# Optimization experiments

Measured on AMD Instinct MI355X. Metric: run time of the kernel, lower is better.

The kernel has to match this reference:

```python
import jax, jax.numpy as jnp
import numpy as np

NT = 128          # num_timesteps (reference query points)
E = 128           # embed_time
H = 128           # nhidden
NH = 1            # num_heads
F = 32            # feature_size
NS = 2            # num_states
EPS = 1e-5


def layer_norm(x, g, b):
    m = jnp.mean(x, axis=-1, keepdims=True)
    v = jnp.mean((x - m) ** 2, axis=-1, keepdims=True)
    return (x - m) * jax.lax.rsqrt(v + EPS) * g + b


def setup_inputs() -> dict:
    key = jax.random.key(0)
    ks = jax.random.split(key, 24)
    nrm = lambda k, s: (jax.random.normal(k, s) * 0.05).astype(jnp.float32)
    inp = {
        "input": jax.random.normal(ks[0], (8, F, 512), dtype=jnp.float32),
        "mask": jax.random.randint(ks[1], (8, F, 512), 0, 2).astype(jnp.float32),
        "timesteps": jnp.sort(jax.random.uniform(ks[2], (8, 512), dtype=jnp.float32), axis=-1),
        # time embedding
        "periodic_w": nrm(ks[3], (E - 1, 1)), "periodic_b": nrm(ks[4], (E - 1,)),
        "lin_w": nrm(ks[5], (1, 1)), "lin_b": nrm(ks[6], (1,)),
        # query / key projections + layer norms
        "q_w": nrm(ks[7], (E, E)), "q_b": nrm(ks[8], (E,)),
        "q_g": jnp.ones((E,), jnp.float32), "q_be": jnp.zeros((E,), jnp.float32),
        "k_w": nrm(ks[9], (E, E)), "k_b": nrm(ks[10], (E,)),
        "k_g": jnp.ones((E,), jnp.float32), "k_be": jnp.zeros((E,), jnp.float32),
        # attention_norm over h*2F channels, then output linear + LN to nhidden
        "attn_g": jnp.ones((NH * 2 * F,), jnp.float32), "attn_b": jnp.zeros((NH * 2 * F,), jnp.float32),
        "out_w": nrm(ks[11], (H, NH * 2 * F)), "out_b": nrm(ks[12], (H,)),
        "out_g": jnp.ones((H,), jnp.float32), "out_be": jnp.zeros((H,), jnp.float32),
        # GRU (torch gate order r, z, n)
        "gru_wih": nrm(ks[13], (3 * H, H)), "gru_whh": nrm(ks[14], (3 * H, H)),
        "gru_bih": nrm(ks[15], (3 * H,)), "gru_bhh": nrm(ks[16], (3 * H,)),
        # classifier MLP
        "c1_w": nrm(ks[17], (H, H)), "c1_b": nrm(ks[18], (H,)),
        "c2_w": nrm(ks[19], (H, H)), "c2_b": nrm(ks[20], (H,)),
        "c3_w": nrm(ks[21], (NS, H)), "c3_b": nrm(ks[22], (NS,)),
    }
    return inp


def time_embedding(tt, lin_w, lin_b, periodic_w, periodic_b):
    t = tt[..., None]                                   # (..., 1)
    out1 = t @ lin_w.T + lin_b                          # (..., 1)
    out2 = jnp.sin(t @ periodic_w.T + periodic_b)       # (..., E-1)
    return jnp.concatenate([out1, out2], axis=-1)       # (..., E)


def reference(input, mask, timesteps, periodic_w, periodic_b, lin_w, lin_b,
              q_w, q_b, q_g, q_be, k_w, k_b, k_g, k_be,
              attn_g, attn_b, out_w, out_b, out_g, out_be,
              gru_wih, gru_whh, gru_bih, gru_bhh,
              c1_w, c1_b, c2_w, c2_b, c3_w, c3_b):
    B = input.shape[0]
    x_in = jnp.transpose(input, (0, 2, 1))              # (B, T, F)
    m = 1.0 - jnp.transpose(mask, (0, 2, 1))            # (B, T, F)
    x_in = x_in * (m > 0).astype(x_in.dtype)
    x = jnp.concatenate([x_in, m], axis=-1)             # (B, T, 2F)
    mk = jnp.concatenate([m, m], axis=-1)               # (B, T, 2F)

    key_e = time_embedding(timesteps, lin_w, lin_b, periodic_w, periodic_b)        # (B, T, E)
    qtimes = jnp.linspace(0.0, 1.0, NT)
    query_e = time_embedding(qtimes[None], lin_w, lin_b, periodic_w, periodic_b)   # (1, NT, E)

    q = layer_norm(query_e @ q_w.T + q_b, q_g, q_be)    # (1, NT, E)
    k = layer_norm(key_e @ k_w.T + k_b, k_g, k_be)      # (B, T, E)

    etk = E // NH
    q = q.reshape(1, NT, NH, etk).transpose(0, 2, 1, 3)         # (1, h, NT, etk)
    k = k.reshape(B, -1, NH, etk).transpose(0, 2, 1, 3)         # (B, h, T, etk)

    scores = jnp.einsum("ahqd,bhkd->bhqk", q, k) / np.sqrt(etk)  # (B, h, NT, T)
    # per-channel masked softmax over keys: (B, h, NT, T, 2F)
    logits = jnp.where(mk[:, None, None, :, :] == 0, -1e9, scores[..., None])
    p_attn = jax.nn.softmax(logits, axis=-2)
    att = jnp.sum(p_attn * x[:, None, None, :, :], axis=-2)     # (B, h, NT, 2F)

    x2 = att.transpose(0, 2, 1, 3).reshape(B, NT, NH * 2 * F)
    x2 = layer_norm(x2, attn_g, attn_b)
    out = layer_norm(x2 @ out_w.T + out_b, out_g, out_be)       # (B, NT, H)

    # GRU over the NT reference timesteps, last hidden state
    seq = out.transpose(1, 0, 2)                                # (NT, B, H)
    h0 = jnp.zeros((B, H), out.dtype)

    def gru_step(h, x_t):
        gi = x_t @ gru_wih.T + gru_bih
        gh = h @ gru_whh.T + gru_bhh
        ir, iz, inn = jnp.split(gi, 3, axis=-1)
        hr, hz, hn = jnp.split(gh, 3, axis=-1)
        r = jax.nn.sigmoid(ir + hr)
        z = jax.nn.sigmoid(iz + hz)
        n = jnp.tanh(inn + r * hn)
        h_new = (1.0 - z) * n + z * h
        return h_new, None

    h_last, _ = jax.lax.scan(gru_step, h0, seq)

    h1 = jax.nn.relu(h_last @ c1_w.T + c1_b)
    h2 = jax.nn.relu(h1 @ c2_w.T + c2_b)
    return h2 @ c3_w.T + c3_b                                   # (B, num_states) logits
```

## Files before the change

kernel.cpp:

```cpp
#include <hip/hip_runtime.h>
#include <math.h>

#define LN_EPS 1e-5f

typedef _Float16 h2v __attribute__((ext_vector_type(2)));

__device__ __forceinline__ float dot4(float4 a, float4 b) {
    return a.x*b.x + a.y*b.y + a.z*b.z + a.w*b.w;
}
__device__ __forceinline__ float fast_sigmoid(float x) {
    return 1.f / (1.f + __expf(-x));
}
__device__ __forceinline__ float fast_tanh(float x) {
    const float e = __expf(2.f * x);
    return 1.f - 2.f / (e + 1.f);
}
__device__ __forceinline__ float fdot2u(unsigned int a, unsigned int b, float c) {
#if __has_builtin(__builtin_amdgcn_fdot2)
    return __builtin_amdgcn_fdot2(__builtin_bit_cast(h2v, a),
                                  __builtin_bit_cast(h2v, b), c, false);
#else
    const h2v av = __builtin_bit_cast(h2v, a);
    const h2v bv = __builtin_bit_cast(h2v, b);
    return c + (float)av[0]*(float)bv[0] + (float)av[1]*(float)bv[1];
#endif
}
__device__ __forceinline__ float wsum64(float v) {
    #pragma unroll
    for (int off = 32; off > 0; off >>= 1) v += __shfl_xor(v, off);
    return v;
}

__global__ void k_embed_proj(
    const float* __restrict__ input, const float* __restrict__ mask,
    const float* __restrict__ timesteps,
    const float* __restrict__ pw, const float* __restrict__ pb,
    const float* __restrict__ lw, const float* __restrict__ lb,
    const float* __restrict__ q_w, const float* __restrict__ q_b,
    const float* __restrict__ q_g, const float* __restrict__ q_be,
    const float* __restrict__ k_w, const float* __restrict__ k_b,
    const float* __restrict__ k_g, const float* __restrict__ k_be,
    float* __restrict__ qs, float* __restrict__ kT, float2* __restrict__ xm)
{
    const int blk = blockIdx.x;
    const int tid = threadIdx.x;

    __shared__ __align__(16) float e[4][128];
    __shared__ __align__(16) float4 red[128];
    __shared__ __align__(16) float proj[4][128];
    __shared__ __align__(16) float2 tile[32][65];

    if (blk >= 1056) {
        const int b  = blk - 1056;
        const int cg = tid >> 6;
        const int tt = tid & 63;
        for (int t0 = 0; t0 < 512; t0 += 64) {
            for (int c16 = 0; c16 < 16; ++c16) {
                const int c = c16*2 + cg;
                const float m = mask [(size_t)(b*32 + c)*512 + t0 + tt];
                const float x = input[(size_t)(b*32 + c)*512 + t0 + tt];
                const float mm = 1.0f - m;
                tile[c][tt] = make_float2(x*mm, mm);
            }
            __syncthreads();
            const int c2 = tid & 31;
            const int tg = tid >> 5;
            #pragma unroll
            for (int k = 0; k < 16; ++k) {
                const int t = tg*16 + k;
                xm[((size_t)b*512 + t0 + t)*32 + c2] = tile[c2][t];
            }
            __syncthreads();
        }
        return;
    }

    const bool isq = blk < 32;
    float tv[4];
    int kidx0 = 0;
    if (isq) {
        const int q0 = blk * 4;
        #pragma unroll
        for (int r = 0; r < 4; ++r) tv[r] = (float)(q0 + r) * (1.0f/127.0f);
    } else {
        kidx0 = (blk - 32) * 4;
        #pragma unroll
        for (int r = 0; r < 4; ++r) tv[r] = timesteps[kidx0 + r];
    }

    float pwj = 0.f, pbj = 0.f;
    if (tid > 0) { pwj = pw[tid-1]; pbj = pb[tid-1]; }
    const float lw0 = lw[0], lb0 = lb[0];
    #pragma unroll
    for (int r = 0; r < 4; ++r)
        e[r][tid] = (tid == 0) ? (tv[r]*lw0 + lb0) : sinf(tv[r]*pwj + pbj);
    __syncthreads();

    const float* W  = isq ? q_w  : k_w;
    const float* Bv = isq ? q_b  : k_b;
    const float* G  = isq ? q_g  : k_g;
    const float* Be = isq ? q_be : k_be;

    {
        const int jj = tid >> 2, dc = tid & 3;
        const float4* e0 = (const float4*)(&e[0][0]);
        const float4* e1 = (const float4*)(&e[1][0]);
        const float4* e2 = (const float4*)(&e[2][0]);
        const float4* e3 = (const float4*)(&e[3][0]);
        #pragma unroll
        for (int jb = 0; jb < 4; ++jb) {
            const int j = jb*32 + jj;
            const float4* wrow = (const float4*)(W + (size_t)j*128);
            float a0=0.f, a1=0.f, a2=0.f, a3=0.f;
            #pragma unroll
            for (int k = 0; k < 8; ++k) {
                const int idx = dc + 4*k;
                const float4 w4 = wrow[idx];
                a0 += dot4(w4, e0[idx]);
                a1 += dot4(w4, e1[idx]);
                a2 += dot4(w4, e2[idx]);
                a3 += dot4(w4, e3[idx]);
            }
            a0 += __shfl_xor(a0, 1, 4); a0 += __shfl_xor(a0, 2, 4);
            a1 += __shfl_xor(a1, 1, 4); a1 += __shfl_xor(a1, 2, 4);
            a2 += __shfl_xor(a2, 1, 4); a2 += __shfl_xor(a2, 2, 4);
            a3 += __shfl_xor(a3, 1, 4); a3 += __shfl_xor(a3, 2, 4);
            if (dc == 0) {
                const float bj = Bv[j];
                proj[0][j] = a0 + bj; proj[1][j] = a1 + bj;
                proj[2][j] = a2 + bj; proj[3][j] = a3 + bj;
            }
        }
    }
    __syncthreads();

    float acc[4];
    #pragma unroll
    for (int r = 0; r < 4; ++r) acc[r] = proj[r][tid];

    red[tid] = make_float4(acc[0], acc[1], acc[2], acc[3]);
    __syncthreads();
    for (int s = 64; s > 0; s >>= 1) {
        if (tid < s) {
            float4 m = red[tid]; const float4 o = red[tid+s];
            m.x += o.x; m.y += o.y; m.z += o.z; m.w += o.w;
            red[tid] = m;
        }
        __syncthreads();
    }
    float4 mean = red[0];
    mean.x *= (1.0f/128.0f); mean.y *= (1.0f/128.0f);
    mean.z *= (1.0f/128.0f); mean.w *= (1.0f/128.0f);
    __syncthreads();
    const float d0 = acc[0]-mean.x, d1 = acc[1]-mean.y,
                d2 = acc[2]-mean.z, d3 = acc[3]-mean.w;
    red[tid] = make_float4(d0*d0, d1*d1, d2*d2, d3*d3);
    __syncthreads();
    for (int s = 64; s > 0; s >>= 1) {
        if (tid < s) {
            float4 m = red[tid]; const float4 o = red[tid+s];
            m.x += o.x; m.y += o.y; m.z += o.z; m.w += o.w;
            red[tid] = m;
        }
        __syncthreads();
    }
    float4 var = red[0];
    var.x *= (1.0f/128.0f); var.y *= (1.0f/128.0f);
    var.z *= (1.0f/128.0f); var.w *= (1.0f/128.0f);

    const float gg = G[tid], bb = Be[tid];
    const float o0 = d0*rsqrtf(var.x+LN_EPS)*gg + bb;
    const float o1 = d1*rsqrtf(var.y+LN_EPS)*gg + bb;
    const float o2 = d2*rsqrtf(var.z+LN_EPS)*gg + bb;
    const float o3 = d3*rsqrtf(var.w+LN_EPS)*gg + bb;

    if (isq) {
        const float sc = 0.08838834764831845f;
        const int q0 = blk*4;
        qs[(size_t)(q0+0)*128 + tid] = o0*sc;
        qs[(size_t)(q0+1)*128 + tid] = o1*sc;
        qs[(size_t)(q0+2)*128 + tid] = o2*sc;
        qs[(size_t)(q0+3)*128 + tid] = o3*sc;
    } else {
        const int b = kidx0 >> 9;
        const int t = kidx0 & 511;
        *(float4*)(kT + ((size_t)(b*128 + tid))*512 + t) =
            make_float4(o0, o1, o2, o3);
    }
}

__global__ void __launch_bounds__(256) k_attn(
    const float2* __restrict__ xm,
    const float* __restrict__ qs, const float* __restrict__ kT,
    const float* __restrict__ attn_g, const float* __restrict__ attn_b,
    const float* __restrict__ out_w, const float* __restrict__ out_b,
    const float* __restrict__ out_g, const float* __restrict__ out_be,
    float* __restrict__ outm)
{
    const int b     = blockIdx.x >> 5;
    const int qbase = (blockIdx.x & 31) * 4;
    const int tid   = threadIdx.x;

    __shared__ __align__(16) float et[4][512];
    __shared__ __align__(16) float qsh[4][128];
    __shared__ __align__(16) float wsh[128*66];
    __shared__ __align__(16) float sA[4][8][32];
    __shared__ __align__(16) float aA[4][8][32];
    __shared__ __align__(16) float x2s[4][64];
    __shared__ float redC[4];

    for (int idx = tid; idx < 512; idx += 256)
        qsh[idx >> 7][idx & 127] = qs[(size_t)(qbase + (idx >> 7))*128 + (idx & 127)];
    for (int idx = tid; idx < 8192; idx += 256)
        wsh[(idx >> 6)*66 + (idx & 63)] = out_w[idx];
    __syncthreads();

    {
        const int grp = tid >> 7;
        const int tl  = tid & 127;
        const int q0  = grp*2;
        const float4* kp = (const float4*)kT + (size_t)b*128*128 + tl;
        float4 a0 = make_float4(0,0,0,0), a1 = make_float4(0,0,0,0);
        for (int d = 0; d < 128; ++d) {
            const float4 kv = kp[(size_t)d*128];
            const float qa = qsh[q0][d], qb = qsh[q0+1][d];
            a0.x += qa*kv.x; a0.y += qa*kv.y; a0.z += qa*kv.z; a0.w += qa*kv.w;
            a1.x += qb*kv.x; a1.y += qb*kv.y; a1.z += qb*kv.z; a1.w += qb*kv.w;
        }
        a0.x = __expf(a0.x); a0.y = __expf(a0.y); a0.z = __expf(a0.z); a0.w = __expf(a0.w);
        a1.x = __expf(a1.x); a1.y = __expf(a1.y); a1.z = __expf(a1.z); a1.w = __expf(a1.w);
        ((float4*)et[q0])[tl]   = a0;
        ((float4*)et[q0+1])[tl] = a1;
    }
    __syncthreads();

    {
        const int c   = tid & 31;
        const int seg = tid >> 5;
        const float2* xp = xm + ((size_t)b*512 + seg*64)*32 + c;
        float s0=0,s1=0,s2=0,s3=0, a0=0,a1=0,a2=0,a3=0;
        #pragma unroll 4
        for (int i = 0; i < 64; ++i) {
            const float2 v = xp[(size_t)i*32];
            const int t = seg*64 + i;
            const float w0 = et[0][t]*v.y, w1 = et[1][t]*v.y;
            const float w2 = et[2][t]*v.y, w3 = et[3][t]*v.y;
            s0 += w0; s1 += w1; s2 += w2; s3 += w3;
            a0 += w0*v.x; a1 += w1*v.x; a2 += w2*v.x; a3 += w3*v.x;
        }
        sA[0][seg][c]=s0; sA[1][seg][c]=s1; sA[2][seg][c]=s2; sA[3][seg][c]=s3;
        aA[0][seg][c]=a0; aA[1][seg][c]=a1; aA[2][seg][c]=a2; aA[3][seg][c]=a3;
    }
    __syncthreads();

    {
        const int ql = tid >> 6;
        const int c2 = tid & 63;
        const int cc = c2 & 31;
        float ss = 0.f;
        #pragma unroll
        for (int g = 0; g < 8; ++g) ss += sA[ql][g][cc];
        float attv;
        if (c2 < 32) {
            float aa = 0.f;
            #pragma unroll
            for (int g = 0; g < 8; ++g) aa += aA[ql][g][cc];
            attv = (ss > 0.f) ? aa/ss : 0.f;
        } else {
            attv = (ss > 0.f) ? 1.0f : 0.0f;
        }
        const float mean = wsum64(attv) * (1.0f/64.0f);
        const float dv = attv - mean;
        const float var = wsum64(dv*dv) * (1.0f/64.0f);
        x2s[ql][c2] = dv*rsqrtf(var+LN_EPS)*attn_g[c2] + attn_b[c2];
    }
    __syncthreads();

    {
        const int jhalf = tid >> 7;
        const int j     = tid & 127;
        const int wave  = tid >> 6;
        for (int lq2 = 0; lq2 < 2; ++lq2) {
            const int ql = jhalf*2 + lq2;
            float acc = out_b[j];
            const float4* wrow = (const float4*)(wsh + j*66);
            const float4* xr   = (const float4*)x2s[ql];
            #pragma unroll
            for (int k = 0; k < 16; ++k) acc += dot4(wrow[k], xr[k]);

            float v = wsum64(acc);
            if ((tid & 63) == 0) redC[wave] = v;
            __syncthreads();
            const float mean = (redC[jhalf*2] + redC[jhalf*2+1]) * (1.0f/128.0f);
            __syncthreads();
            const float d = acc - mean;
            v = wsum64(d*d);
            if ((tid & 63) == 0) redC[wave] = v;
            __syncthreads();
            const float var = (redC[jhalf*2] + redC[jhalf*2+1]) * (1.0f/128.0f);
            outm[((size_t)b*128 + qbase + ql)*128 + j] =
                d*rsqrtf(var+LN_EPS)*out_g[j] + out_be[j];
            __syncthreads();
        }
    }
}

__global__ void k_gi(const float* __restrict__ outm,
                     const float* __restrict__ wih, const float* __restrict__ bih,
                     float* __restrict__ gi)
{
    const int qi  = blockIdx.x;
    const int tid = threadIdx.x;
    __shared__ __align__(16) float rows[8][128];
    for (int idx = tid; idx < 1024; idx += 384) {
        const int b = idx >> 7, d = idx & 127;
        rows[b][d] = outm[(size_t)(b*128+qi)*128 + d];
    }
    __syncthreads();

    const int g0 = tid >> 2, dc = tid & 3;
    #pragma unroll
    for (int gb = 0; gb < 4; ++gb) {
        const int g = gb*96 + g0;
        const float4* wrow = (const float4*)(wih + (size_t)g*128);
        float acc[8] = {0,0,0,0,0,0,0,0};
        #pragma unroll
        for (int k = 0; k < 8; ++k) {
            const int idx = dc + 4*k;
            const float4 w4 = wrow[idx];
            #pragma unroll
            for (int b = 0; b < 8; ++b)
                acc[b] += dot4(w4, ((const float4*)rows[b])[idx]);
        }
        #pragma unroll
        for (int b = 0; b < 8; ++b) {
            acc[b] += __shfl_xor(acc[b], 1, 4);
            acc[b] += __shfl_xor(acc[b], 2, 4);
        }
        if (dc == 0) {
            const float bi = bih[g];
            #pragma unroll
            for (int b = 0; b < 8; ++b)
                gi[((size_t)qi*8 + b)*384 + g] = acc[b] + bi;
        }
    }
}

__global__ void __launch_bounds__(512) k_gru_cls(
    const float* __restrict__ gi,
    const float* __restrict__ whh, const float* __restrict__ bhh,
    const float* __restrict__ c1w, const float* __restrict__ c1b,
    const float* __restrict__ c2w, const float* __restrict__ c2b,
    const float* __restrict__ c3w, const float* __restrict__ c3b,
    float* __restrict__ out)
{
    const int b   = blockIdx.x;
    const int tid = threadIdx.x;
    const int s   = tid >> 7;
    const int u   = tid & 127;

    __shared__ __align__(16) unsigned int lds[25344];
    unsigned int* hP  = lds;
    float* part = (float*)&lds[64];
    float* hcls = (float*)&lds[1216];

    {
        const float4* w4 = (const float4*)whh;
        #pragma unroll 4
        for (int k = 0; k < 24; ++k) {
            const int idx = tid + k*512;
            const float4 v = w4[idx];
            const int row = idx >> 5, c4 = idx & 31;
            h2v p0; p0[0] = (_Float16)v.x; p0[1] = (_Float16)v.y;
            h2v p1; p1[0] = (_Float16)v.z; p1[1] = (_Float16)v.w;
            lds[row*66 + c4*2    ] = __builtin_bit_cast(unsigned int, p0);
            lds[row*66 + c4*2 + 1] = __builtin_bit_cast(unsigned int, p1);
        }
    }
    __syncthreads();

    unsigned int wreg[3][16];
    #pragma unroll
    for (int g = 0; g < 3; ++g) {
        const uint2* src = (const uint2*)&lds[(g*128 + u)*66 + 16*s];
        #pragma unroll
        for (int i = 0; i < 8; ++i) {
            const uint2 t = src[i];
            wreg[g][2*i] = t.x; wreg[g][2*i+1] = t.y;
        }
    }
    __syncthreads();

    const float* gbase = gi + (size_t)b*384;
    float bh_r=0.f, bh_z=0.f, bh_n=0.f, gr0=0.f, gz0=0.f, gn0=0.f, hprev=0.f;
    if (tid < 64) hP[tid] = 0u;
    if (s == 0) {
        bh_r = bhh[u]; bh_z = bhh[u+128]; bh_n = bhh[u+256];
        gr0 = gbase[u]; gz0 = gbase[u+128]; gn0 = gbase[u+256];
    }
    __syncthreads();

    for (int qi = 0; qi < 128; ++qi) {
        const uint4* hp4 = (const uint4*)hP + s*4;
        float ar = 0.f, az = 0.f, an = 0.f;
        #pragma unroll
        for (int i = 0; i < 4; ++i) {
            const uint4 hv = hp4[i];
            ar = fdot2u(wreg[0][4*i+0], hv.x, ar);
            ar = fdot2u(wreg[0][4*i+1], hv.y, ar);
            ar = fdot2u(wreg[0][4*i+2], hv.z, ar);
            ar = fdot2u(wreg[0][4*i+3], hv.w, ar);
            az = fdot2u(wreg[1][4*i+0], hv.x, az);
            az = fdot2u(wreg[1][4*i+1], hv.y, az);
            az = fdot2u(wreg[1][4*i+2], hv.z, az);
            az = fdot2u(wreg[1][4*i+3], hv.w, az);
            an = fdot2u(wreg[2][4*i+0], hv.x, an);
            an = fdot2u(wreg[2][4*i+1], hv.y, an);
            an = fdot2u(wreg[2][4*i+2], hv.z, an);
            an = fdot2u(wreg[2][4*i+3], hv.w, an);
        }
        if (s > 0) {
            float* p = part + (s-1)*384;
            p[u] = ar; p[u+128] = az; p[u+256] = an;
        }

        float grn=0.f, gzn=0.f, gnn=0.f;
        if (s == 0 && qi < 127) {
            const float* gb = gbase + (size_t)(qi+1)*3072;
            grn = gb[u]; gzn = gb[u+128]; gnn = gb[u+256];
        }
        __syncthreads();

        if (s == 0) {
            const float ghr = ar + part[u]     + part[384+u]     + part[768+u]     + bh_r;
            const float ghz = az + part[128+u] + part[384+128+u] + part[768+128+u] + bh_z;
            const float ghn = an + part[256+u] + part[384+256+u] + part[768+256+u] + bh_n;
            const float r = fast_sigmoid(gr0 + ghr);
            const float z = fast_sigmoid(gz0 + ghz);
            const float n = fast_tanh(gn0 + r*ghn);
            const float hn2 = (1.f - z)*n + z*hprev;
            hprev = hn2;
            gr0 = grn; gz0 = gzn; gn0 = gnn;
            const float other = __shfl_xor(hn2, 1);
            if ((u & 1) == 0) {
                h2v hp; hp[0] = (_Float16)hn2; hp[1] = (_Float16)other;
                hP[u >> 1] = __builtin_bit_cast(unsigned int, hp);
            }
        }
        __syncthreads();
    }

    if (s == 0) hcls[u] = hprev;
    __syncthreads();
    if (tid < 128) {
        float acc = c1b[u];
        const float4* wc = (const float4*)(c1w + (size_t)u*128);
        const float4* v  = (const float4*)hcls;
        #pragma unroll
        for (int d4 = 0; d4 < 32; ++d4) acc += dot4(wc[d4], v[d4]);
        part[u] = fmaxf(acc, 0.f);
    }
    __syncthreads();
    if (tid < 128) {
        float acc = c2b[u];
        const float4* wc = (const float4*)(c2w + (size_t)u*128);
        const float4* v  = (const float4*)part;
        #pragma unroll
        for (int d4 = 0; d4 < 32; ++d4) acc += dot4(wc[d4], v[d4]);
        part[384 + u] = fmaxf(acc, 0.f);
    }
    __syncthreads();
    if (tid < 2) {
        float acc = c3b[tid];
        const float4* wc = (const float4*)(c3w + (size_t)tid*128);
        const float4* v  = (const float4*)(part + 384);
        #pragma unroll
        for (int d4 = 0; d4 < 32; ++d4) acc += dot4(wc[d4], v[d4]);
        out[(size_t)b*2 + tid] = acc;
    }
}

extern "C" void kernel_launch(void* const* d_in, const int* in_sizes, int n_in,
                              void* d_out, int out_size, void* d_ws, size_t ws_size,
                              hipStream_t stream)
{
    const float* input     = (const float*)d_in[0];
    const float* mask      = (const float*)d_in[1];
    const float* timesteps = (const float*)d_in[2];
    const float* pw        = (const float*)d_in[3];
    const float* pb        = (const float*)d_in[4];
    const float* lw        = (const float*)d_in[5];
    const float* lb        = (const float*)d_in[6];
    const float* q_w       = (const float*)d_in[7];
    const float* q_b       = (const float*)d_in[8];
    const float* q_g       = (const float*)d_in[9];
    const float* q_be      = (const float*)d_in[10];
    const float* k_w       = (const float*)d_in[11];
    const float* k_b       = (const float*)d_in[12];
    const float* k_g       = (const float*)d_in[13];
    const float* k_be      = (const float*)d_in[14];
    const float* attn_g    = (const float*)d_in[15];
    const float* attn_b    = (const float*)d_in[16];
    const float* out_w     = (const float*)d_in[17];
    const float* out_b     = (const float*)d_in[18];
    const float* out_g     = (const float*)d_in[19];
    const float* out_be    = (const float*)d_in[20];
    const float* gru_wih   = (const float*)d_in[21];
    const float* gru_whh   = (const float*)d_in[22];
    const float* gru_bih   = (const float*)d_in[23];
    const float* gru_bhh   = (const float*)d_in[24];
    const float* c1_w      = (const float*)d_in[25];
    const float* c1_b      = (const float*)d_in[26];
    const float* c2_w      = (const float*)d_in[27];
    const float* c2_b      = (const float*)d_in[28];
    const float* c3_w      = (const float*)d_in[29];
    const float* c3_b      = (const float*)d_in[30];

    float* ws   = (float*)d_ws;
    float*  qs   = ws;
    float*  kT   = qs   + 16384;
    float*  outm = kT   + 524288;
    float*  gi   = outm + 131072;
    float2* xm   = (float2*)(gi + 393216);

    k_embed_proj<<<1064, 128, 0, stream>>>(input, mask, timesteps,
                                           pw, pb, lw, lb,
                                           q_w, q_b, q_g, q_be,
                                           k_w, k_b, k_g, k_be, qs, kT, xm);
    k_attn<<<256, 256, 0, stream>>>(xm, qs, kT,
                                    attn_g, attn_b, out_w, out_b,
                                    out_g, out_be, outm);
    k_gi<<<128, 384, 0, stream>>>(outm, gru_wih, gru_bih, gi);
    k_gru_cls<<<8, 512, 0, stream>>>(gi, gru_whh, gru_bhh,
                                     c1_w, c1_b, c2_w, c2_b, c3_w, c3_b,
                                     (float*)d_out);
}
```

Measured before the change: 262.5 us.

## Split mask transpose across blocks, prefetch K in scores, pack GRU partials

```diff
diff --git a/kernel.cpp b/kernel.cpp
--- a/kernel.cpp
+++ b/kernel.cpp
@@ -8,12 +8,17 @@
 __device__ __forceinline__ float dot4(float4 a, float4 b) {
     return a.x*b.x + a.y*b.y + a.z*b.z + a.w*b.w;
 }
+__device__ __forceinline__ void fma4(float4& a, float s, float4 v) {
+    a.x += s*v.x; a.y += s*v.y; a.z += s*v.z; a.w += s*v.w;
+}
+__device__ __forceinline__ float fast_rcp(float x) {
+    return __builtin_amdgcn_rcpf(x);
+}
 __device__ __forceinline__ float fast_sigmoid(float x) {
-    return 1.f / (1.f + __expf(-x));
+    return fast_rcp(1.f + __expf(-x));
 }
 __device__ __forceinline__ float fast_tanh(float x) {
-    const float e = __expf(2.f * x);
-    return 1.f - 2.f / (e + 1.f);
+    return 1.f - 2.f*fast_rcp(__expf(2.f*x) + 1.f);
 }
 __device__ __forceinline__ float fdot2u(unsigned int a, unsigned int b, float c) {
 #if __has_builtin(__builtin_amdgcn_fdot2)
@@ -50,40 +55,39 @@
     __shared__ __align__(16) float proj[4][128];
     __shared__ __align__(16) float2 tile[32][65];
 
-    if (blk >= 1056) {
-        const int b  = blk - 1056;
+    if (blk < 64) {
+        const int b  = blk >> 3;
+        const int t0 = (blk & 7) * 64;
         const int cg = tid >> 6;
         const int tt = tid & 63;
-        for (int t0 = 0; t0 < 512; t0 += 64) {
-            for (int c16 = 0; c16 < 16; ++c16) {
-                const int c = c16*2 + cg;
-                const float m = mask [(size_t)(b*32 + c)*512 + t0 + tt];
-                const float x = input[(size_t)(b*32 + c)*512 + t0 + tt];
-                const float mm = 1.0f - m;
-                tile[c][tt] = make_float2(x*mm, mm);
-            }
-            __syncthreads();
-            const int c2 = tid & 31;
-            const int tg = tid >> 5;
-            #pragma unroll
-            for (int k = 0; k < 16; ++k) {
-                const int t = tg*16 + k;
-                xm[((size_t)b*512 + t0 + t)*32 + c2] = tile[c2][t];
-            }
-            __syncthreads();
+        #pragma unroll
+        for (int c16 = 0; c16 < 16; ++c16) {
+            const int c = c16*2 + cg;
+            const float m = mask [(size_t)(b*32 + c)*512 + t0 + tt];
+            const float x = input[(size_t)(b*32 + c)*512 + t0 + tt];
+            const float mm = 1.0f - m;
+            tile[c][tt] = make_float2(x*mm, mm);
+        }
+        __syncthreads();
+        const int c2 = tid & 31;
+        const int tg = tid >> 5;
+        #pragma unroll
+        for (int k = 0; k < 16; ++k) {
+            const int t = tg*16 + k;
+            xm[((size_t)b*512 + t0 + t)*32 + c2] = tile[c2][t];
         }
         return;
     }
 
-    const bool isq = blk < 32;
+    const bool isq = blk < 96;
     float tv[4];
     int kidx0 = 0;
     if (isq) {
-        const int q0 = blk * 4;
+        const int q0 = (blk - 64) * 4;
         #pragma unroll
         for (int r = 0; r < 4; ++r) tv[r] = (float)(q0 + r) * (1.0f/127.0f);
     } else {
-        kidx0 = (blk - 32) * 4;
+        kidx0 = (blk - 96) * 4;
         #pragma unroll
         for (int r = 0; r < 4; ++r) tv[r] = timesteps[kidx0 + r];
     }
@@ -176,7 +180,7 @@
 
     if (isq) {
         const float sc = 0.08838834764831845f;
-        const int q0 = blk*4;
+        const int q0 = (blk - 64)*4;
         qs[(size_t)(q0+0)*128 + tid] = o0*sc;
         qs[(size_t)(q0+1)*128 + tid] = o1*sc;
         qs[(size_t)(q0+2)*128 + tid] = o2*sc;
@@ -219,13 +223,23 @@
         const int grp = tid >> 7;
         const int tl  = tid & 127;
         const int q0  = grp*2;
-        const float4* kp = (const float4*)kT + (size_t)b*128*128 + tl;
+        const float4* kp  = (const float4*)kT + (size_t)b*128*128 + tl;
+        const float4* qa4 = (const float4*)qsh[q0];
+        const float4* qb4 = (const float4*)qsh[q0+1];
         float4 a0 = make_float4(0,0,0,0), a1 = make_float4(0,0,0,0);
-        for (int d = 0; d < 128; ++d) {
-            const float4 kv = kp[(size_t)d*128];
-            const float qa = qsh[q0][d], qb = qsh[q0+1][d];
-            a0.x += qa*kv.x; a0.y += qa*kv.y; a0.z += qa*kv.z; a0.w += qa*kv.w;
-            a1.x += qb*kv.x; a1.y += qb*kv.y; a1.z += qb*kv.z; a1.w += qb*kv.w;
+        float4 c0 = kp[0], c1 = kp[128], c2 = kp[256], c3 = kp[384];
+        for (int c = 0; c < 32; ++c) {
+            float4 n0, n1, n2, n3;
+            if (c < 31) {
+                const float4* kn = kp + (size_t)(4*c+4)*128;
+                n0 = kn[0]; n1 = kn[128]; n2 = kn[256]; n3 = kn[384];
+            }
+            const float4 qa = qa4[c], qb = qb4[c];
+            fma4(a0, qa.x, c0); fma4(a1, qb.x, c0);
+            fma4(a0, qa.y, c1); fma4(a1, qb.y, c1);
+            fma4(a0, qa.z, c2); fma4(a1, qb.z, c2);
+            fma4(a0, qa.w, c3); fma4(a1, qb.w, c3);
+            c0 = n0; c1 = n1; c2 = n2; c3 = n3;
         }
         a0.x = __expf(a0.x); a0.y = __expf(a0.y); a0.z = __expf(a0.z); a0.w = __expf(a0.w);
         a1.x = __expf(a1.x); a1.y = __expf(a1.y); a1.z = __expf(a1.z); a1.w = __expf(a1.w);
@@ -360,9 +374,9 @@
     const int u   = tid & 127;
 
     __shared__ __align__(16) unsigned int lds[25344];
-    unsigned int* hP  = lds;
-    float* part = (float*)&lds[64];
-    float* hcls = (float*)&lds[1216];
+    unsigned int* hP = lds;
+    float4* part4 = (float4*)&lds[64];
+    float* hcls = (float*)&lds[64 + 1536];
 
     {
         const float4* w4 = (const float4*)whh;
@@ -419,10 +433,7 @@
             an = fdot2u(wreg[2][4*i+2], hv.z, an);
             an = fdot2u(wreg[2][4*i+3], hv.w, an);
         }
-        if (s > 0) {
-            float* p = part + (s-1)*384;
-            p[u] = ar; p[u+128] = az; p[u+256] = an;
-        }
+        if (s > 0) part4[(s-1)*128 + u] = make_float4(ar, az, an, 0.f);
 
         float grn=0.f, gzn=0.f, gnn=0.f;
         if (s == 0 && qi < 127) {
@@ -432,9 +443,10 @@
         __syncthreads();
 
         if (s == 0) {
-            const float ghr = ar + part[u]     + part[384+u]     + part[768+u]     + bh_r;
-            const float ghz = az + part[128+u] + part[384+128+u] + part[768+128+u] + bh_z;
-            const float ghn = an + part[256+u] + part[384+256+u] + part[768+256+u] + bh_n;
+            const float4 p0 = part4[u], p1 = part4[128+u], p2 = part4[256+u];
+            const float ghr = ar + p0.x + p1.x + p2.x + bh_r;
+            const float ghz = az + p0.y + p1.y + p2.y + bh_z;
+            const float ghn = an + p0.z + p1.z + p2.z + bh_n;
             const float r = fast_sigmoid(gr0 + ghr);
             const float z = fast_sigmoid(gz0 + ghz);
             const float n = fast_tanh(gn0 + r*ghn);
@@ -450,6 +462,7 @@
         __syncthreads();
     }
 
+    float* scr = (float*)part4;
     if (s == 0) hcls[u] = hprev;
     __syncthreads();
     if (tid < 128) {
@@ -458,22 +471,22 @@
         const float4* v  = (const float4*)hcls;
         #pragma unroll
         for (int d4 = 0; d4 < 32; ++d4) acc += dot4(wc[d4], v[d4]);
-        part[u] = fmaxf(acc, 0.f);
+        scr[u] = fmaxf(acc, 0.f);
     }
     __syncthreads();
     if (tid < 128) {
         float acc = c2b[u];
         const float4* wc = (const float4*)(c2w + (size_t)u*128);
-        const float4* v  = (const float4*)part;
+        const float4* v  = (const float4*)scr;
         #pragma unroll
         for (int d4 = 0; d4 < 32; ++d4) acc += dot4(wc[d4], v[d4]);
-        part[384 + u] = fmaxf(acc, 0.f);
+        scr[128 + u] = fmaxf(acc, 0.f);
     }
     __syncthreads();
     if (tid < 2) {
         float acc = c3b[tid];
         const float4* wc = (const float4*)(c3w + (size_t)tid*128);
-        const float4* v  = (const float4*)(part + 384);
+        const float4* v  = (const float4*)(scr + 128);
         #pragma unroll
         for (int d4 = 0; d4 < 32; ++d4) acc += dot4(wc[d4], v[d4]);
         out[(size_t)b*2 + tid] = acc;
@@ -523,7 +536,7 @@
     float*  gi   = outm + 131072;
     float2* xm   = (float2*)(gi + 393216);
 
-    k_embed_proj<<<1064, 128, 0, stream>>>(input, mask, timesteps,
+    k_embed_proj<<<1120, 128, 0, stream>>>(input, mask, timesteps,
                                            pw, pb, lw, lb,
                                            q_w, q_b, q_g, q_be,
                                            k_w, k_b, k_g, k_be, qs, kT, xm);
```

After: 240.5 us. 1.09x faster.
